# Performance work log

Hardware: AMD Instinct MI355X
Metric: run time of the kernel (lower is better)

Reference implementation:

```python
import jax, jax.numpy as jnp
import numpy as np

C = 256
GROUPS = 8
EPS_GN = 1e-5
EPS_ATTN = 1e-6


def setup_inputs() -> dict:
    key = jax.random.key(0)
    ks = jax.random.split(key, 10)
    b, c, h, w = 8, C, 128, 128
    # xavier_uniform for 1x1 conv weight [out, in]: limit = sqrt(6/(in+out))
    lim = float(np.sqrt(6.0 / (c + c)))
    mkw = lambda k: jax.random.uniform(k, (c, c), jnp.float32, -lim, lim)
    return {
        "x": jax.random.normal(ks[0], (b, c, h, w), jnp.float32),
        "gamma": jnp.ones((c,), jnp.float32),
        "beta": jnp.zeros((c,), jnp.float32),
        "Wq": mkw(ks[1]), "bq": jnp.zeros((c,), jnp.float32),
        "Wk": mkw(ks[2]), "bk": jnp.zeros((c,), jnp.float32),
        "Wv": mkw(ks[3]), "bv": jnp.zeros((c,), jnp.float32),
        "Wp": mkw(ks[4]), "bp": jnp.zeros((c,), jnp.float32),
    }


def _group_norm(x, gamma, beta):
    b, c, h, w = x.shape
    xg = x.reshape(b, GROUPS, c // GROUPS, h, w)
    mean = xg.mean(axis=(2, 3, 4), keepdims=True)
    var = xg.var(axis=(2, 3, 4), keepdims=True)
    xn = ((xg - mean) * jax.lax.rsqrt(var + EPS_GN)).reshape(b, c, h, w)
    return xn * gamma[None, :, None, None] + beta[None, :, None, None]


def _conv1x1(x, W, bias):
    # 1x1 conv == per-pixel matmul: [b,c,h,w] x [o,c] -> [b,o,h,w]
    return jnp.einsum('bchw,oc->bohw', x, W) + bias[None, :, None, None]


def reference(x, gamma, beta, Wq, bq, Wk, bk, Wv, bv, Wp, bp):
    b, c, h, w = x.shape
    xn = _group_norm(x, gamma, beta)
    q = jax.nn.elu(_conv1x1(xn, Wq, bq)) + 1.0
    k = jax.nn.elu(_conv1x1(xn, Wk, bk)) + 1.0
    v = _conv1x1(xn, Wv, bv)
    n = h * w
    q = q.reshape(b, c, n)
    k = k.reshape(b, c, n)
    v = v.reshape(b, c, n)
    kv = jnp.einsum('bcn,bdn->bcd', k, v)          # k @ v^T, [b,c,c]
    k_sum = jnp.sum(k, axis=2, keepdims=True)       # [b,c,1]
    kv = kv / (k_sum + EPS_ATTN)
    out = jnp.einsum('bcd,bdn->bcn', kv, q).reshape(b, c, h, w)
    out = _conv1x1(out, Wp, bp)
    return out + x
```

## Files before the change

### kernel.cpp

```cpp
#include <hip/hip_runtime.h>

typedef unsigned short u16;
using bf16x8 = __attribute__((ext_vector_type(8))) __bf16;
using f32x4  = __attribute__((ext_vector_type(4))) float;

#define BATCH 8
#define CH    256
#define NPIX  16384
#define GN_EPS   1e-5f
#define ATTN_EPS 1e-6f

__device__ __forceinline__ u16 f2bf(float f) {
  unsigned int u = __float_as_uint(f);
  u += 0x7fffu + ((u >> 16) & 1u);
  return (u16)(u >> 16);
}

__global__ void conv_w_kernel(const float* __restrict__ Wq, const float* __restrict__ Wk,
                              const float* __restrict__ Wv,
                              u16* __restrict__ oq, u16* __restrict__ ok, u16* __restrict__ ov) {
  int i = blockIdx.x * 256 + threadIdx.x;
  oq[i] = f2bf(Wq[i]);
  ok[i] = f2bf(Wk[i]);
  ov[i] = f2bf(Wv[i]);
}

__global__ void stats_kernel(const float* __restrict__ x, float* __restrict__ sum,
                             float* __restrict__ sqs) {
  const int gi = blockIdx.x >> 3;
  const int sp = blockIdx.x & 7;
  const float4* p = (const float4*)x + (size_t)gi * 131072 + (size_t)sp * 16384;
  float s = 0.f, ss = 0.f;
  for (int i = 0; i < 64; ++i) {
    float4 v = p[threadIdx.x + i * 256];
    s  += v.x + v.y + v.z + v.w;
    ss += v.x * v.x + v.y * v.y + v.z * v.z + v.w * v.w;
  }
  for (int off = 32; off; off >>= 1) {
    s  += __shfl_xor(s, off);
    ss += __shfl_xor(ss, off);
  }
  __shared__ float rs[4], rss[4];
  const int wave = threadIdx.x >> 6, lane = threadIdx.x & 63;
  if (!lane) { rs[wave] = s; rss[wave] = ss; }
  __syncthreads();
  if (!threadIdx.x) {
    atomicAdd(&sum[gi], rs[0] + rs[1] + rs[2] + rs[3]);
    atomicAdd(&sqs[gi], rss[0] + rss[1] + rss[2] + rss[3]);
  }
}

__global__ void finalize_kernel(const float* __restrict__ sums, const float* __restrict__ sqs,
                                const float* __restrict__ gamma, const float* __restrict__ beta,
                                float* __restrict__ sA, float* __restrict__ sB) {
  const int t = blockIdx.x * 256 + threadIdx.x;
  const int c = t & 255;
  const int gi = (t >> 8) * 8 + (c >> 5);
  const float inv = 1.f / 524288.f;
  const float mean = sums[gi] * inv;
  const float var = sqs[gi] * inv - mean * mean;
  const float rstd = rsqrtf(var + GN_EPS);
  const float a = rstd * gamma[c];
  sA[t] = a;
  sB[t] = beta[c] - mean * a;
}

__global__ __launch_bounds__(1024, 4) void fused_kv_kernel(
    const float* __restrict__ x, const u16* __restrict__ Wkb, const u16* __restrict__ Wvb,
    const float* __restrict__ bk, const float* __restrict__ bv,
    const float* __restrict__ sA, const float* __restrict__ sB,
    float* __restrict__ ksum, float* __restrict__ KV) {
  __shared__ __align__(16) u16 xnv[64 * 288];
  __shared__ __align__(16) u16 Kcp[256 * 72];

  const int b = blockIdx.x >> 5;
  const int sp = blockIdx.x & 31;
  const int tid = threadIdx.x;
  const int wave = tid >> 6;
  const int lane = tid & 63;
  const int m = lane & 15;
  const int q = lane >> 4;

  const int ctg = wave & 7;
  const int ptg = wave >> 3;
  const int ckg = wave >> 2;
  const int cvg = wave & 3;

  const float* xb = x + (size_t)b * CH * NPIX;
  const float* sAb = sA + b * CH;
  const float* sBb = sB + b * CH;

  f32x4 accKV[4][4];
#pragma unroll
  for (int i = 0; i < 4; ++i)
#pragma unroll
    for (int j = 0; j < 4; ++j) accKV[i][j] = {0.f, 0.f, 0.f, 0.f};
  float ksum_acc = 0.f;

  const int p_ = tid & 63;
  const int cq = tid >> 6;

  for (int ch = 0; ch < 8; ++ch) {
    const int pix0 = sp * 512 + ch * 64;
    __syncthreads();
#pragma unroll
    for (int i = 0; i < 4; ++i) {
      const int c = (cq + 16 * i) * 4;
      const float v0 = xb[(size_t)(c + 0) * NPIX + pix0 + p_] * sAb[c + 0] + sBb[c + 0];
      const float v1 = xb[(size_t)(c + 1) * NPIX + pix0 + p_] * sAb[c + 1] + sBb[c + 1];
      const float v2 = xb[(size_t)(c + 2) * NPIX + pix0 + p_] * sAb[c + 2] + sBb[c + 2];
      const float v3 = xb[(size_t)(c + 3) * NPIX + pix0 + p_] * sAb[c + 3] + sBb[c + 3];
      const unsigned int lo = (unsigned int)f2bf(v0) | ((unsigned int)f2bf(v1) << 16);
      const unsigned int hi = (unsigned int)f2bf(v2) | ((unsigned int)f2bf(v3) << 16);
      *(uint2*)&xnv[p_ * 288 + c] = make_uint2(lo, hi);
    }
    __syncthreads();

    f32x4 ac[2][2];
#pragma unroll
    for (int i = 0; i < 2; ++i)
#pragma unroll
      for (int pp = 0; pp < 2; ++pp) ac[i][pp] = {0.f, 0.f, 0.f, 0.f};
#pragma unroll
    for (int ks = 0; ks < 8; ++ks) {
      const bf16x8 a0 = *(const bf16x8*)(Wkb + ((2 * ctg + 0) * 16 + m) * 256 + ks * 32 + q * 8);
      const bf16x8 a1 = *(const bf16x8*)(Wkb + ((2 * ctg + 1) * 16 + m) * 256 + ks * 32 + q * 8);
#pragma unroll
      for (int pp = 0; pp < 2; ++pp) {
        const bf16x8 bfr = *(const bf16x8*)&xnv[((2 * ptg + pp) * 16 + m) * 288 + ks * 32 + q * 8];
        ac[0][pp] = __builtin_amdgcn_mfma_f32_16x16x32_bf16(a0, bfr, ac[0][pp], 0, 0, 0);
        ac[1][pp] = __builtin_amdgcn_mfma_f32_16x16x32_bf16(a1, bfr, ac[1][pp], 0, 0, 0);
      }
    }
#pragma unroll
    for (int i = 0; i < 2; ++i) {
#pragma unroll
      for (int r = 0; r < 4; ++r) {
        const int row = (2 * ctg + i) * 16 + q * 4 + r;
        const float bias = bk[row];
#pragma unroll
        for (int pp = 0; pp < 2; ++pp) {
          float v = ac[i][pp][r] + bias;
          v = v > 0.f ? v + 1.f : __expf(v);
          Kcp[row * 72 + (2 * ptg + pp) * 16 + m] = f2bf(v);
        }
      }
    }

    f32x4 av[2][2];
#pragma unroll
    for (int i = 0; i < 2; ++i)
#pragma unroll
      for (int pp = 0; pp < 2; ++pp) av[i][pp] = {0.f, 0.f, 0.f, 0.f};
#pragma unroll
    for (int ks = 0; ks < 8; ++ks) {
      const bf16x8 a0 = *(const bf16x8*)(Wvb + ((2 * ctg + 0) * 16 + m) * 256 + ks * 32 + q * 8);
      const bf16x8 a1 = *(const bf16x8*)(Wvb + ((2 * ctg + 1) * 16 + m) * 256 + ks * 32 + q * 8);
#pragma unroll
      for (int pp = 0; pp < 2; ++pp) {
        const bf16x8 bfr = *(const bf16x8*)&xnv[((2 * ptg + pp) * 16 + m) * 288 + ks * 32 + q * 8];
        av[0][pp] = __builtin_amdgcn_mfma_f32_16x16x32_bf16(a0, bfr, av[0][pp], 0, 0, 0);
        av[1][pp] = __builtin_amdgcn_mfma_f32_16x16x32_bf16(a1, bfr, av[1][pp], 0, 0, 0);
      }
    }
    __syncthreads();
    u16* Vcp = xnv;
#pragma unroll
    for (int i = 0; i < 2; ++i) {
#pragma unroll
      for (int r = 0; r < 4; ++r) {
        const int row = (2 * ctg + i) * 16 + q * 4 + r;
        const float bias = bv[row];
#pragma unroll
        for (int pp = 0; pp < 2; ++pp)
          Vcp[row * 72 + (2 * ptg + pp) * 16 + m] = f2bf(av[i][pp][r] + bias);
      }
    }
    __syncthreads();

    {
      const int krow = tid & 255;
      const int kseg = tid >> 8;
      const bf16x8 k0 = *(const bf16x8*)&Kcp[krow * 72 + kseg * 16];
      const bf16x8 k1 = *(const bf16x8*)&Kcp[krow * 72 + kseg * 16 + 8];
      float s = 0.f;
#pragma unroll
      for (int j = 0; j < 8; ++j) s += (float)k0[j] + (float)k1[j];
      ksum_acc += s;
    }

#pragma unroll
    for (int ks = 0; ks < 2; ++ks) {
      bf16x8 af[4], bfv[4];
#pragma unroll
      for (int i = 0; i < 4; ++i)
        af[i] = *(const bf16x8*)&Kcp[((4 * ckg + i) * 16 + m) * 72 + ks * 32 + q * 8];
#pragma unroll
      for (int j = 0; j < 4; ++j)
        bfv[j] = *(const bf16x8*)&Vcp[((4 * cvg + j) * 16 + m) * 72 + ks * 32 + q * 8];
#pragma unroll
      for (int i = 0; i < 4; ++i)
#pragma unroll
        for (int j = 0; j < 4; ++j)
          accKV[i][j] = __builtin_amdgcn_mfma_f32_16x16x32_bf16(af[i], bfv[j], accKV[i][j], 0, 0, 0);
    }
  }

  atomicAdd(&ksum[b * CH + (tid & 255)], ksum_acc);
  float* KVb = KV + (size_t)b * CH * CH;
#pragma unroll
  for (int i = 0; i < 4; ++i)
#pragma unroll
    for (int j = 0; j < 4; ++j)
#pragma unroll
      for (int r = 0; r < 4; ++r) {
        const int row = (4 * ckg + i) * 16 + q * 4 + r;
        const int col = (4 * cvg + j) * 16 + m;
        atomicAdd(&KVb[row * CH + col], accKV[i][j][r]);
      }
}

__global__ __launch_bounds__(256) void m_kernel(const float* __restrict__ Wp,
                                                const float* __restrict__ KV,
                                                const float* __restrict__ ksum,
                                                u16* __restrict__ Mb) {
  __shared__ float WpL[16 * 256];
  const int b = blockIdx.x >> 4;
  const int rt = blockIdx.x & 15;
  const int tid = threadIdx.x;
#pragma unroll
  for (int i = 0; i < 16; ++i) WpL[i * 256 + tid] = Wp[(rt * 16 + i) * 256 + tid];
  __syncthreads();
  float acc[16];
#pragma unroll
  for (int r = 0; r < 16; ++r) acc[r] = 0.f;
  const float* KVb = KV + (size_t)b * 65536;
  const float* ksb = ksum + b * 256;
  for (int k = 0; k < 256; ++k) {
    const float rs = 1.f / (ksb[k] + ATTN_EPS);
    const float v = KVb[k * 256 + tid] * rs;
#pragma unroll
    for (int r = 0; r < 16; ++r) acc[r] += WpL[r * 256 + k] * v;
  }
#pragma unroll
  for (int r = 0; r < 16; ++r) Mb[(size_t)b * 65536 + (rt * 16 + r) * 256 + tid] = f2bf(acc[r]);
}

__global__ __launch_bounds__(256, 4) void out_kernel(
    const float* __restrict__ x, const u16* __restrict__ Wqb, const float* __restrict__ bq,
    const float* __restrict__ sA, const float* __restrict__ sB, const u16* __restrict__ Mb,
    const float* __restrict__ bp, float* __restrict__ out) {
  __shared__ __align__(16) u16 xn2[64 * 288];
  __shared__ __align__(16) u16 qpc[64 * 288];
  const int b = blockIdx.x >> 8;
  const int pix0 = (blockIdx.x & 255) * 64;
  const int tid = threadIdx.x;
  const int wave = tid >> 6;
  const int lane = tid & 63;
  const int m = lane & 15;
  const int q = lane >> 4;

  const float* xb = x + (size_t)b * CH * NPIX;
  const float* sAb = sA + b * CH;
  const float* sBb = sB + b * CH;

  const int p_ = tid & 63;
  const int cq = tid >> 6;
#pragma unroll
  for (int i = 0; i < 16; ++i) {
    const int c = (cq + 4 * i) * 4;
    const float v0 = xb[(size_t)(c + 0) * NPIX + pix0 + p_] * sAb[c + 0] + sBb[c + 0];
    const float v1 = xb[(size_t)(c + 1) * NPIX + pix0 + p_] * sAb[c + 1] + sBb[c + 1];
    const float v2 = xb[(size_t)(c + 2) * NPIX + pix0 + p_] * sAb[c + 2] + sBb[c + 2];
    const float v3 = xb[(size_t)(c + 3) * NPIX + pix0 + p_] * sAb[c + 3] + sBb[c + 3];
    const unsigned int lo = (unsigned int)f2bf(v0) | ((unsigned int)f2bf(v1) << 16);
    const unsigned int hi = (unsigned int)f2bf(v2) | ((unsigned int)f2bf(v3) << 16);
    *(uint2*)&xn2[p_ * 288 + c] = make_uint2(lo, hi);
  }
  __syncthreads();

  f32x4 aq[4][4];
#pragma unroll
  for (int pt = 0; pt < 4; ++pt)
#pragma unroll
    for (int ct = 0; ct < 4; ++ct) aq[pt][ct] = {0.f, 0.f, 0.f, 0.f};
#pragma unroll
  for (int ks = 0; ks < 8; ++ks) {
    bf16x8 af[4];
#pragma unroll
    for (int pt = 0; pt < 4; ++pt)
      af[pt] = *(const bf16x8*)&xn2[(pt * 16 + m) * 288 + ks * 32 + q * 8];
#pragma unroll
    for (int ct = 0; ct < 4; ++ct) {
      const bf16x8 bfr = *(const bf16x8*)(Wqb + ((4 * wave + ct) * 16 + m) * 256 + ks * 32 + q * 8);
#pragma unroll
      for (int pt = 0; pt < 4; ++pt)
        aq[pt][ct] = __builtin_amdgcn_mfma_f32_16x16x32_bf16(af[pt], bfr, aq[pt][ct], 0, 0, 0);
    }
  }
#pragma unroll
  for (int ct = 0; ct < 4; ++ct) {
    const int c2 = (4 * wave + ct) * 16 + m;
    const float bias = bq[c2];
#pragma unroll
    for (int pt = 0; pt < 4; ++pt)
#pragma unroll
      for (int r = 0; r < 4; ++r) {
        float v = aq[pt][ct][r] + bias;
        v = v > 0.f ? v + 1.f : __expf(v);
        qpc[(pt * 16 + q * 4 + r) * 288 + c2] = f2bf(v);
      }
  }
  __syncthreads();

  f32x4 ao[4][4];
#pragma unroll
  for (int ct = 0; ct < 4; ++ct)
#pragma unroll
    for (int pt = 0; pt < 4; ++pt) ao[ct][pt] = {0.f, 0.f, 0.f, 0.f};
  const u16* Ab = Mb + (size_t)b * 65536;
#pragma unroll
  for (int ks = 0; ks < 8; ++ks) {
    bf16x8 af2[4];
#pragma unroll
    for (int ct = 0; ct < 4; ++ct)
      af2[ct] = *(const bf16x8*)(Ab + ((4 * wave + ct) * 16 + m) * 256 + ks * 32 + q * 8);
#pragma unroll
    for (int pt = 0; pt < 4; ++pt) {
      const bf16x8 bfr = *(const bf16x8*)&qpc[(pt * 16 + m) * 288 + ks * 32 + q * 8];
#pragma unroll
      for (int ct = 0; ct < 4; ++ct)
        ao[ct][pt] = __builtin_amdgcn_mfma_f32_16x16x32_bf16(af2[ct], bfr, ao[ct][pt], 0, 0, 0);
    }
  }
  float* ob = out + (size_t)b * CH * NPIX;
#pragma unroll
  for (int ct = 0; ct < 4; ++ct)
#pragma unroll
    for (int r = 0; r < 4; ++r) {
      const int row = (4 * wave + ct) * 16 + q * 4 + r;
      const float bias = bp[row];
#pragma unroll
      for (int pt = 0; pt < 4; ++pt) {
        const int idx = row * NPIX + pix0 + pt * 16 + m;
        ob[idx] = ao[ct][pt][r] + bias + xb[idx];
      }
    }
}

extern "C" void kernel_launch(void* const* d_in, const int* in_sizes, int n_in,
                              void* d_out, int out_size, void* d_ws, size_t ws_size,
                              hipStream_t stream) {
  const float* x     = (const float*)d_in[0];
  const float* gamma = (const float*)d_in[1];
  const float* beta  = (const float*)d_in[2];
  const float* Wq    = (const float*)d_in[3];
  const float* bq    = (const float*)d_in[4];
  const float* Wk    = (const float*)d_in[5];
  const float* bk    = (const float*)d_in[6];
  const float* Wv    = (const float*)d_in[7];
  const float* bv    = (const float*)d_in[8];
  const float* Wp    = (const float*)d_in[9];
  const float* bp    = (const float*)d_in[10];
  float* out = (float*)d_out;

  float* wsf  = (float*)d_ws;
  float* sum  = wsf;
  float* sqs  = wsf + 64;
  float* ksum = wsf + 128;
  float* KV   = wsf + 2176;
  float* sA   = wsf + 526464;
  float* sB   = wsf + 528512;
  u16* Wqb = (u16*)(wsf + 530560);
  u16* Wkb = Wqb + 65536;
  u16* Wvb = Wkb + 65536;
  u16* Mb  = Wvb + 65536;

  hipMemsetAsync(wsf, 0, (size_t)526464 * sizeof(float), stream);
  conv_w_kernel<<<256, 256, 0, stream>>>(Wq, Wk, Wv, Wqb, Wkb, Wvb);
  stats_kernel<<<512, 256, 0, stream>>>(x, sum, sqs);
  finalize_kernel<<<8, 256, 0, stream>>>(sum, sqs, gamma, beta, sA, sB);
  fused_kv_kernel<<<256, 1024, 0, stream>>>(x, Wkb, Wvb, bk, bv, sA, sB, ksum, KV);
  m_kernel<<<128, 256, 0, stream>>>(Wp, KV, ksum, Mb);
  out_kernel<<<2048, 256, 0, stream>>>(x, Wqb, bq, sA, sB, Mb, bp, out);
}
```

Before: 728.1 us.

## Replace KV atomic accumulation with per-block partials plus reduction kernel; share LDS buffer

When workspace is large enough, each fused_kv block writes its 256x256 KV partial to its own slot instead of doing global float atomics. A new kv_reduce kernel then sums the 32 partials per batch. This avoids contention from atomics (each of 32 blocks per batch hits the same addresses) and shrinks the memset, at the cost of an extra 64MB write and read pass. Separately, out_kernel reuses one LDS buffer for xn and q, with an added barrier, halving its shared memory to allow more occupancy.

```diff
diff --git a/kernel.cpp b/kernel.cpp
--- a/kernel.cpp
+++ b/kernel.cpp
@@ -69,7 +69,7 @@
     const float* __restrict__ x, const u16* __restrict__ Wkb, const u16* __restrict__ Wvb,
     const float* __restrict__ bk, const float* __restrict__ bv,
     const float* __restrict__ sA, const float* __restrict__ sB,
-    float* __restrict__ ksum, float* __restrict__ KV) {
+    float* __restrict__ ksum, float* __restrict__ kvdst, int mode) {
   __shared__ __align__(16) u16 xnv[64 * 288];
   __shared__ __align__(16) u16 Kcp[256 * 72];
 
@@ -207,17 +207,47 @@
   }
 
   atomicAdd(&ksum[b * CH + (tid & 255)], ksum_acc);
-  float* KVb = KV + (size_t)b * CH * CH;
-#pragma unroll
-  for (int i = 0; i < 4; ++i)
-#pragma unroll
-    for (int j = 0; j < 4; ++j)
-#pragma unroll
-      for (int r = 0; r < 4; ++r) {
-        const int row = (4 * ckg + i) * 16 + q * 4 + r;
-        const int col = (4 * cvg + j) * 16 + m;
-        atomicAdd(&KVb[row * CH + col], accKV[i][j][r]);
-      }
+  if (mode == 0) {
+    float* KVp = kvdst + (size_t)blockIdx.x * 65536;
+#pragma unroll
+    for (int i = 0; i < 4; ++i)
+#pragma unroll
+      for (int j = 0; j < 4; ++j)
+#pragma unroll
+        for (int r = 0; r < 4; ++r) {
+          const int row = (4 * ckg + i) * 16 + q * 4 + r;
+          const int col = (4 * cvg + j) * 16 + m;
+          KVp[row * CH + col] = accKV[i][j][r];
+        }
+  } else {
+    float* KVb = kvdst + (size_t)b * 65536;
+#pragma unroll
+    for (int i = 0; i < 4; ++i)
+#pragma unroll
+      for (int j = 0; j < 4; ++j)
+#pragma unroll
+        for (int r = 0; r < 4; ++r) {
+          const int row = (4 * ckg + i) * 16 + q * 4 + r;
+          const int col = (4 * cvg + j) * 16 + m;
+          atomicAdd(&KVb[row * CH + col], accKV[i][j][r]);
+        }
+  }
+}
+
+__global__ __launch_bounds__(256) void kv_reduce_kernel(const float* __restrict__ kvpart,
+                                                        float* __restrict__ KV) {
+  const int base = blockIdx.x * 1024 + threadIdx.x;
+#pragma unroll
+  for (int i = 0; i < 4; ++i) {
+    const int e = base + i * 256;
+    const int b = e >> 16;
+    const int rc = e & 65535;
+    const float* p = kvpart + (size_t)(b * 32) * 65536 + rc;
+    float s = 0.f;
+#pragma unroll 8
+    for (int j = 0; j < 32; ++j) s += p[(size_t)j * 65536];
+    KV[e] = s;
+  }
 }
 
 __global__ __launch_bounds__(256) void m_kernel(const float* __restrict__ Wp,
@@ -250,8 +280,7 @@
     const float* __restrict__ x, const u16* __restrict__ Wqb, const float* __restrict__ bq,
     const float* __restrict__ sA, const float* __restrict__ sB, const u16* __restrict__ Mb,
     const float* __restrict__ bp, float* __restrict__ out) {
-  __shared__ __align__(16) u16 xn2[64 * 288];
-  __shared__ __align__(16) u16 qpc[64 * 288];
+  __shared__ __align__(16) u16 buf[64 * 288];
   const int b = blockIdx.x >> 8;
   const int pix0 = (blockIdx.x & 255) * 64;
   const int tid = threadIdx.x;
@@ -275,7 +304,7 @@
     const float v3 = xb[(size_t)(c + 3) * NPIX + pix0 + p_] * sAb[c + 3] + sBb[c + 3];
     const unsigned int lo = (unsigned int)f2bf(v0) | ((unsigned int)f2bf(v1) << 16);
     const unsigned int hi = (unsigned int)f2bf(v2) | ((unsigned int)f2bf(v3) << 16);
-    *(uint2*)&xn2[p_ * 288 + c] = make_uint2(lo, hi);
+    *(uint2*)&buf[p_ * 288 + c] = make_uint2(lo, hi);
   }
   __syncthreads();
 
@@ -289,7 +318,7 @@
     bf16x8 af[4];
 #pragma unroll
     for (int pt = 0; pt < 4; ++pt)
-      af[pt] = *(const bf16x8*)&xn2[(pt * 16 + m) * 288 + ks * 32 + q * 8];
+      af[pt] = *(const bf16x8*)&buf[(pt * 16 + m) * 288 + ks * 32 + q * 8];
 #pragma unroll
     for (int ct = 0; ct < 4; ++ct) {
       const bf16x8 bfr = *(const bf16x8*)(Wqb + ((4 * wave + ct) * 16 + m) * 256 + ks * 32 + q * 8);
@@ -298,6 +327,7 @@
         aq[pt][ct] = __builtin_amdgcn_mfma_f32_16x16x32_bf16(af[pt], bfr, aq[pt][ct], 0, 0, 0);
     }
   }
+  __syncthreads();
 #pragma unroll
   for (int ct = 0; ct < 4; ++ct) {
     const int c2 = (4 * wave + ct) * 16 + m;
@@ -308,7 +338,7 @@
       for (int r = 0; r < 4; ++r) {
         float v = aq[pt][ct][r] + bias;
         v = v > 0.f ? v + 1.f : __expf(v);
-        qpc[(pt * 16 + q * 4 + r) * 288 + c2] = f2bf(v);
+        buf[(pt * 16 + q * 4 + r) * 288 + c2] = f2bf(v);
       }
   }
   __syncthreads();
@@ -327,7 +357,7 @@
       af2[ct] = *(const bf16x8*)(Ab + ((4 * wave + ct) * 16 + m) * 256 + ks * 32 + q * 8);
 #pragma unroll
     for (int pt = 0; pt < 4; ++pt) {
-      const bf16x8 bfr = *(const bf16x8*)&qpc[(pt * 16 + m) * 288 + ks * 32 + q * 8];
+      const bf16x8 bfr = *(const bf16x8*)&buf[(pt * 16 + m) * 288 + ks * 32 + q * 8];
 #pragma unroll
       for (int ct = 0; ct < 4; ++ct)
         ao[ct][pt] = __builtin_amdgcn_mfma_f32_16x16x32_bf16(af2[ct], bfr, ao[ct][pt], 0, 0, 0);
@@ -376,11 +406,16 @@
   u16* Wvb = Wkb + 65536;
   u16* Mb  = Wvb + 65536;
 
-  hipMemsetAsync(wsf, 0, (size_t)526464 * sizeof(float), stream);
+  const bool bigws = ws_size >= ((size_t)72 << 20);
+  float* kvpart = bigws ? (wsf + ((size_t)1 << 20)) : KV;
+  const int mode = bigws ? 0 : 1;
+
+  hipMemsetAsync(wsf, 0, (size_t)(bigws ? 2176 : 526464) * sizeof(float), stream);
   conv_w_kernel<<<256, 256, 0, stream>>>(Wq, Wk, Wv, Wqb, Wkb, Wvb);
   stats_kernel<<<512, 256, 0, stream>>>(x, sum, sqs);
   finalize_kernel<<<8, 256, 0, stream>>>(sum, sqs, gamma, beta, sA, sB);
-  fused_kv_kernel<<<256, 1024, 0, stream>>>(x, Wkb, Wvb, bk, bv, sA, sB, ksum, KV);
+  fused_kv_kernel<<<256, 1024, 0, stream>>>(x, Wkb, Wvb, bk, bv, sA, sB, ksum, kvpart, mode);
+  if (bigws) kv_reduce_kernel<<<512, 256, 0, stream>>>(kvpart, KV);
   m_kernel<<<128, 256, 0, stream>>>(Wp, KV, ksum, Mb);
   out_kernel<<<2048, 256, 0, stream>>>(x, Wqb, bq, sA, sB, Mb, bp, out);
 }
```

Result: no change. 726.8 us (-0.2%).
